# Performance work log

Measured on AMD Instinct MI355X. Metric: run time of the kernel, lower is better.

The kernel has to match this reference:

```python
import jax, jax.numpy as jnp
import numpy as np

# Static graph layout: B equal-sized graphs so per-graph k is constant (jit-friendly).
NUM_GRAPHS = 128
NODES_PER_GRAPH = 1024
NUM_NODES = NUM_GRAPHS * NODES_PER_GRAPH  # 131072
NUM_EDGES = NUM_NODES * 32               # 4194304
CHANNELS = 256
RATIO = 0.5
K = max(1, int(NODES_PER_GRAPH * RATIO))  # 512, matches max(1, int(count*ratio))


def setup_inputs() -> dict:
    key = jax.random.key(0)
    k0, k1, k2, k3 = jax.random.split(key, 4)
    x = jax.random.normal(k0, (NUM_NODES, CHANNELS), dtype=jnp.float32)
    edge_index = jax.random.randint(k1, (2, NUM_EDGES), 0, NUM_NODES, dtype=jnp.int64)
    batch = (jnp.arange(NUM_NODES, dtype=jnp.int64) // NODES_PER_GRAPH)
    # score MLP params: Linear(C, C) -> tanh -> Linear(C, 1)
    s = 1.0 / np.sqrt(CHANNELS)
    W1 = jax.random.uniform(k2, (CHANNELS, CHANNELS), jnp.float32, -s, s)
    b1 = jnp.zeros((CHANNELS,), jnp.float32)
    W2 = jax.random.uniform(k3, (CHANNELS, 1), jnp.float32, -s, s)
    b2 = jnp.zeros((1,), jnp.float32)
    return {"x": x, "edge_index": edge_index, "batch": batch,
            "W1": W1, "b1": b1, "W2": W2, "b2": b2}


def reference(x, edge_index, batch, W1, b1, W2, b2):
    # Note: SAGPool.forward computes a GNN score then discards it and calls
    # super().forward, which recomputes scores with the self.score MLP. The GNN
    # path is dead code (and would error in torch); the effective math is below.
    scores = (jnp.tanh(x @ W1 + b1) @ W2 + b2)[:, 0]  # [num_nodes]

    # Per-graph top-k, vectorized across all graphs (equal-sized segments).
    s = scores.reshape(NUM_GRAPHS, NODES_PER_GRAPH)
    top_s, top_i = jax.lax.top_k(s, K)  # descending per graph, matches torch.topk
    offsets = (jnp.arange(NUM_GRAPHS, dtype=top_i.dtype) * NODES_PER_GRAPH)[:, None]
    perm = (top_i + offsets).reshape(-1)  # [B*K] global indices, graphs in order

    x_pooled = x[perm]
    batch_pooled = batch[perm]
    scores_pooled = top_s.reshape(-1)

    # Edge filtering: keep edges whose both endpoints survive.
    keep = jnp.zeros((NUM_NODES,), dtype=bool).at[perm].set(True)
    row, col = edge_index
    edge_mask = keep[row] & keep[col]
    # Static-shape compaction: stable-sort kept edges to the front, pad with -1.
    order = jnp.argsort(~edge_mask, stable=True)
    edge_index_pooled = jnp.where(edge_mask[order][None, :], edge_index[:, order], -1)

    return x_pooled, edge_index_pooled, batch_pooled, perm, scores_pooled
```

## Files before the change

kernel.cpp:

```cpp
#include <hip/hip_runtime.h>
#include <hip/hip_bf16.h>

#define NG 128
#define NPG 1024
#define NN (NG * NPG)
#define NE (NN * 32)
#define CH 256
#define KSEL 512

#define CAP 128
#define EPS 0.02f

#define OUT_X      0
#define OUT_EDGE   16777216
#define OUT_BATCH  25165824
#define OUT_PERM   25231360
#define OUT_SCORES 25296896

#define WS_SCORES  0
#define WS_KEEP    524288
#define WS_COUNTS  540672
#define WS_OFFSETS 544768
#define WS_BFRAG   548864
#define WS_BIDX    679936
#define WS_BSCORE  745472
#define WS_BN      811008
#define WS_BLO     811520

typedef __attribute__((ext_vector_type(8))) short bf16x8;
typedef __attribute__((ext_vector_type(4))) float f32x4;

__device__ __forceinline__ unsigned short f2bf(float f) {
    unsigned int b = __float_as_uint(f);
    return (unsigned short)((b + 0x7fffu + ((b >> 16) & 1u)) >> 16);
}

__device__ __forceinline__ float tanh_fast(float h) {
    const float e = __expf(2.0f * h);
    return 1.0f - 2.0f / (e + 1.0f);
}

__global__ __launch_bounds__(256)
void k_cvtW(const float* __restrict__ W1, unsigned short* __restrict__ W1b,
            unsigned int* __restrict__ keep_bits)
{
    const int t = blockIdx.x * 256 + threadIdx.x;
    if (t < NN / 32) keep_bits[t] = 0u;
    const int s    = t >> 10;
    const int rem  = t & 1023;
    const int n    = rem >> 6;
    const int lane = rem & 63;
    const int kbase = s * 32 + (lane >> 4) * 8;
    const int col   = n * 16 + (lane & 15);
    unsigned short u[8];
    #pragma unroll
    for (int j = 0; j < 8; ++j)
        u[j] = f2bf(W1[(size_t)(kbase + j) * CH + col]);
    uint4 v;
    v.x = u[0] | ((unsigned int)u[1] << 16);
    v.y = u[2] | ((unsigned int)u[3] << 16);
    v.z = u[4] | ((unsigned int)u[5] << 16);
    v.w = u[6] | ((unsigned int)u[7] << 16);
    *(uint4*)&W1b[(size_t)t * 8] = v;
}

__global__ __launch_bounds__(256, 3)
void k_mfma_scores(const float* __restrict__ x, const unsigned short* __restrict__ W1b,
                   const float* __restrict__ b1, const float* __restrict__ W2,
                   const float* __restrict__ b2, float* __restrict__ scores)
{
    __shared__ __align__(16) float Xf[2][2048];
    __shared__ float epi[4][64];

    const int tid = threadIdx.x;
    const int w_  = tid >> 6;
    const int l   = tid & 63;
    const int n0  = blockIdx.x * 64;

    #define STAGEX(c_, b_)                                                          \
    do {                                                                            \
        _Pragma("unroll")                                                           \
        for (int i = 0; i < 2; ++i) {                                               \
            const int G   = i * 256 + tid;                  \
            const int row = G >> 3;                                                 \
            const int gl  = (G & 7) ^ (row & 7);        \
            const float* src = x + (size_t)(n0 + row) * CH + (c_) * 32 + gl * 4;    \
            float* lb = &Xf[b_][0] + i * 1024 + w_ * 256;    \
            __builtin_amdgcn_global_load_lds(                                       \
                (const __attribute__((address_space(1))) void*)src,                 \
                (__attribute__((address_space(3))) void*)lb, 16, 0, 0);             \
        }                                                                           \
    } while (0)

    f32x4 acc[4][4];
    #pragma unroll
    for (int m = 0; m < 4; ++m)
        #pragma unroll
        for (int n = 0; n < 4; ++n)
            acc[m][n] = (f32x4){0.f, 0.f, 0.f, 0.f};

    const unsigned short* Wl = W1b + l * 8;
    bf16x8 bc[4], bn[4];
    #pragma unroll
    for (int ni = 0; ni < 4; ++ni)
        bc[ni] = *(const bf16x8*)&Wl[(size_t)(w_ * 4 + ni) * 512];

    STAGEX(0, 0);
    __syncthreads();

    #pragma unroll
    for (int s = 0; s < 8; ++s) {
        if (s < 7) STAGEX(s + 1, (s + 1) & 1);

        if (s < 7) {
            #pragma unroll
            for (int ni = 0; ni < 4; ++ni)
                bn[ni] = *(const bf16x8*)&Wl[(size_t)((s + 1) * 16 + w_ * 4 + ni) * 512];
        }

        const char* Xc = (const char*)&Xf[s & 1][0];
        bf16x8 a[4];
        #pragma unroll
        for (int m = 0; m < 4; ++m) {
            const int row = m * 16 + (l & 15);
            const int sw  = row & 7;
            const int g0  = (l >> 4) * 2;
            const float4 f0 = *(const float4*)(Xc + row * 128 + ((g0 ^ sw) << 4));
            const float4 f1 = *(const float4*)(Xc + row * 128 + (((g0 + 1) ^ sw) << 4));
            union { bf16x8 v; __hip_bfloat162 h[4]; } ua;
            ua.h[0] = __float22bfloat162_rn(make_float2(f0.x, f0.y));
            ua.h[1] = __float22bfloat162_rn(make_float2(f0.z, f0.w));
            ua.h[2] = __float22bfloat162_rn(make_float2(f1.x, f1.y));
            ua.h[3] = __float22bfloat162_rn(make_float2(f1.z, f1.w));
            a[m] = ua.v;
        }
        #pragma unroll
        for (int ni = 0; ni < 4; ++ni)
            #pragma unroll
            for (int m = 0; m < 4; ++m)
                acc[m][ni] = __builtin_amdgcn_mfma_f32_16x16x32_bf16(a[m], bc[ni], acc[m][ni], 0, 0, 0);
        #pragma unroll
        for (int ni = 0; ni < 4; ++ni) bc[ni] = bn[ni];

        __syncthreads();
    }
    #undef STAGEX

    float part[16];
    #pragma unroll
    for (int i = 0; i < 16; ++i) part[i] = 0.f;
    #pragma unroll
    for (int ni = 0; ni < 4; ++ni) {
        const int col = w_ * 64 + ni * 16 + (l & 15);
        const float b1c = b1[col];
        const float w2c = W2[col];
        #pragma unroll
        for (int m = 0; m < 4; ++m)
            #pragma unroll
            for (int r = 0; r < 4; ++r)
                part[m * 4 + r] += tanh_fast(acc[m][ni][r] + b1c) * w2c;
    }
    #pragma unroll
    for (int off = 1; off < 16; off <<= 1)
        #pragma unroll
        for (int i = 0; i < 16; ++i)
            part[i] += __shfl_xor(part[i], off, 64);

    if ((l & 15) == 0) {
        const int gq = l >> 4;
        #pragma unroll
        for (int m = 0; m < 4; ++m)
            #pragma unroll
            for (int r = 0; r < 4; ++r)
                epi[w_][m * 16 + gq * 4 + r] = part[m * 4 + r];
    }
    __syncthreads();
    if (tid < 64)
        scores[n0 + tid] = epi[0][tid] + epi[1][tid] + epi[2][tid] + epi[3][tid] + b2[0];
}

__global__ __launch_bounds__(512)
void k_topk(const float* __restrict__ scores, float* __restrict__ out,
            unsigned int* __restrict__ keep_bits, int* __restrict__ band_idx,
            int* __restrict__ band_n, int* __restrict__ band_lo)
{
    __shared__ float sv[1024];
    __shared__ int   si[1024];
    __shared__ int   s_lo, s_hi;
    const int g = blockIdx.x;
    const int t = threadIdx.x;
    sv[t]       = scores[g * NPG + t];       si[t]       = t;
    sv[t + 512] = scores[g * NPG + t + 512]; si[t + 512] = t + 512;

    for (int size = 2; size <= 1024; size <<= 1) {
        for (int stride = size >> 1; stride > 0; stride >>= 1) {
            __syncthreads();
            const int lo = ((t & ~(stride - 1)) << 1) | (t & (stride - 1));
            const int hi = lo + stride;
            const bool dirDesc = ((lo & size) == 0);
            const float va = sv[lo], vb = sv[hi];
            const int ia = si[lo], ib = si[hi];
            const bool aB = (va > vb) || (va == vb && ia < ib);
            if (aB != dirDesc) {
                sv[lo] = vb; sv[hi] = va;
                si[lo] = ib; si[hi] = ia;
            }
        }
    }
    __syncthreads();
    if (t == 0) { s_hi = 1024; }
    __syncthreads();
    const float tau = sv[511];
    if (sv[t] <= tau + EPS && (t == 0 || sv[t - 1] > tau + EPS)) s_lo = t;
    {
        const int p2 = t + 512;
        if (sv[p2] < tau - EPS && sv[p2 - 1] >= tau - EPS) s_hi = p2;
    }
    __syncthreads();
    const int lo = s_lo;
    const int bn = min(s_hi - lo, CAP);

    const int gi = g * NPG + si[t];
    out[OUT_BATCH + g * KSEL + t] = (float)g;
    if (t < lo) {
        out[OUT_PERM   + g * KSEL + t] = (float)gi;
        out[OUT_SCORES + g * KSEL + t] = sv[t];
        atomicOr(&keep_bits[gi >> 5], 1u << (gi & 31));
    }
    if (t < CAP)
        band_idx[g * CAP + t] = (t < bn) ? si[lo + t] : 0;
    if (t == 0) { band_n[g] = bn; band_lo[g] = lo; }
}

__global__ __launch_bounds__(256, 2)
void k_rescore(const float* __restrict__ x, const float* __restrict__ W1,
               const float* __restrict__ b1, const float* __restrict__ W2,
               const float* __restrict__ b2, const int* __restrict__ band_idx,
               const int* __restrict__ band_n, float* __restrict__ band_scores)
{
    const int g = blockIdx.x >> 2;
    const int c0 = (blockIdx.x & 3) * 32;
    if (band_n[g] <= c0) return;

    __shared__ __align__(16) float W1s[16][CH];
    __shared__ __align__(16) float Xs[32][16];

    const int tid = threadIdx.x;
    const int w_  = tid >> 6;
    const int l   = tid & 63;

    int iv = 0;
    if (w_ < 2) iv = band_idx[g * CAP + c0 + w_ * 16 + (l >> 2)] & 1023;
    const float* xg = x + ((size_t)g * NPG + iv) * CH;

    const float4 b1v = *(const float4*)&b1[l * 4];
    float acc[8][4];
    #pragma unroll
    for (int n = 0; n < 8; ++n) {
        acc[n][0] = b1v.x; acc[n][1] = b1v.y; acc[n][2] = b1v.z; acc[n][3] = b1v.w;
    }

    for (int kc = 0; kc < 16; ++kc) {
        __syncthreads();
        #pragma unroll
        for (int it = 0; it < 4; ++it) {
            const float* gp = W1 + (size_t)kc * (16 * CH) + (w_ * 4 + it) * CH + l * 4;
            float* lb = &W1s[0][0] + (w_ * 4 + it) * CH;
            __builtin_amdgcn_global_load_lds(
                (const __attribute__((address_space(1))) void*)gp,
                (__attribute__((address_space(3))) void*)lb, 16, 0, 0);
        }
        if (w_ < 2) {
            const float* gp = xg + kc * 16 + (l & 3) * 4;
            float* lb = &Xs[0][0] + w_ * 256;
            __builtin_amdgcn_global_load_lds(
                (const __attribute__((address_space(1))) void*)gp,
                (__attribute__((address_space(3))) void*)lb, 16, 0, 0);
        }
        __syncthreads();

        #pragma unroll
        for (int kq = 0; kq < 4; ++kq) {
            const int k4 = kq * 4;
            const float4 wv0 = *(const float4*)&W1s[k4 + 0][l * 4];
            const float4 wv1 = *(const float4*)&W1s[k4 + 1][l * 4];
            const float4 wv2 = *(const float4*)&W1s[k4 + 2][l * 4];
            const float4 wv3 = *(const float4*)&W1s[k4 + 3][l * 4];
            #pragma unroll
            for (int n = 0; n < 8; ++n) {
                const float4 xv = *(const float4*)&Xs[w_ * 8 + n][k4];
                acc[n][0] = fmaf(xv.x, wv0.x, acc[n][0]);
                acc[n][1] = fmaf(xv.x, wv0.y, acc[n][1]);
                acc[n][2] = fmaf(xv.x, wv0.z, acc[n][2]);
                acc[n][3] = fmaf(xv.x, wv0.w, acc[n][3]);
                acc[n][0] = fmaf(xv.y, wv1.x, acc[n][0]);
                acc[n][1] = fmaf(xv.y, wv1.y, acc[n][1]);
                acc[n][2] = fmaf(xv.y, wv1.z, acc[n][2]);
                acc[n][3] = fmaf(xv.y, wv1.w, acc[n][3]);
                acc[n][0] = fmaf(xv.z, wv2.x, acc[n][0]);
                acc[n][1] = fmaf(xv.z, wv2.y, acc[n][1]);
                acc[n][2] = fmaf(xv.z, wv2.z, acc[n][2]);
                acc[n][3] = fmaf(xv.z, wv2.w, acc[n][3]);
                acc[n][0] = fmaf(xv.w, wv3.x, acc[n][0]);
                acc[n][1] = fmaf(xv.w, wv3.y, acc[n][1]);
                acc[n][2] = fmaf(xv.w, wv3.z, acc[n][2]);
                acc[n][3] = fmaf(xv.w, wv3.w, acc[n][3]);
            }
        }
    }

    const float4 w2v = *(const float4*)&W2[l * 4];
    const float  bb  = b2[0];
    float s_[8];
    #pragma unroll
    for (int n = 0; n < 8; ++n) {
        s_[n] = tanhf(acc[n][0]) * w2v.x + tanhf(acc[n][1]) * w2v.y
              + tanhf(acc[n][2]) * w2v.z + tanhf(acc[n][3]) * w2v.w;
    }
    #pragma unroll
    for (int off = 1; off < 64; off <<= 1)
        #pragma unroll
        for (int n = 0; n < 8; ++n)
            s_[n] += __shfl_xor(s_[n], off, 64);

    if (l == 0) {
        #pragma unroll
        for (int n = 0; n < 8; ++n)
            band_scores[g * CAP + c0 + w_ * 8 + n] = s_[n] + bb;
    }
}

__global__ __launch_bounds__(64)
void k_bandsel(const float* __restrict__ band_scores, const int* __restrict__ band_idx,
               const int* __restrict__ band_n, const int* __restrict__ band_lo,
               float* __restrict__ out, unsigned int* __restrict__ keep_bits)
{
    __shared__ float bs[CAP];
    __shared__ int   bi[CAP];
    const int g = blockIdx.x;
    const int t = threadIdx.x;
    const int n  = band_n[g];
    const int lo = band_lo[g];
    int needed = KSEL - lo;
    if (needed > n) needed = n;

    #pragma unroll
    for (int h = 0; h < 2; ++h) {
        const int q = t + h * 64;
        const bool valid = q < n;
        bs[q] = valid ? band_scores[g * CAP + q] : -3.402823466e+38f;
        bi[q] = valid ? band_idx[g * CAP + q] : (NPG + q);
    }
    __syncthreads();
    for (int size = 2; size <= CAP; size <<= 1) {
        for (int stride = size >> 1; stride > 0; stride >>= 1) {
            __syncthreads();
            const int lo_i = ((t & ~(stride - 1)) << 1) | (t & (stride - 1));
            const int hi_i = lo_i + stride;
            const bool dirDesc = ((lo_i & size) == 0);
            const float va = bs[lo_i], vb = bs[hi_i];
            const int ia = bi[lo_i], ib = bi[hi_i];
            const bool aB = (va > vb) || (va == vb && ia < ib);
            if (aB != dirDesc) {
                bs[lo_i] = vb; bs[hi_i] = va;
                bi[lo_i] = ib; bi[hi_i] = ia;
            }
        }
    }
    __syncthreads();
    #pragma unroll
    for (int h = 0; h < 2; ++h) {
        const int s = t + h * 64;
        if (s < needed) {
            const int li = bi[s];
            const int gi = g * NPG + li;
            out[OUT_PERM   + g * KSEL + lo + s] = (float)gi;
            out[OUT_SCORES + g * KSEL + lo + s] = bs[s];
            atomicOr(&keep_bits[gi >> 5], 1u << (gi & 31));
        }
    }
}

__global__ __launch_bounds__(256)
void k_gather(const float* __restrict__ x, const float* __restrict__ perm_f,
              float* __restrict__ out_x)
{
    const int row  = blockIdx.x * 4 + (threadIdx.x >> 6);
    const int lane = threadIdx.x & 63;
    const int pi = (int)perm_f[row];
    const float4* src = (const float4*)&x[(size_t)pi * CH];
    float4* dst = (float4*)&out_x[(size_t)row * CH];
    dst[lane] = src[lane];
}

__global__ __launch_bounds__(256)
void k_edgecount(const int* __restrict__ ei, const unsigned int* __restrict__ keep_bits,
                 int* __restrict__ counts, float* __restrict__ out_edge)
{
    const int t = threadIdx.x;
    const float4 neg = make_float4(-1.f, -1.f, -1.f, -1.f);
    #pragma unroll
    for (int q = 0; q < 4; ++q) {
        ((float4*)out_edge)[(size_t)blockIdx.x * 1024 + q * 256 + t] = neg;
        ((float4*)(out_edge + NE))[(size_t)blockIdx.x * 1024 + q * 256 + t] = neg;
    }

    const size_t base = (size_t)blockIdx.x * 4096 + (size_t)t * 16;
    const int* rowp = ei;
    const int* colp = ei + NE;
    int rv[16], cv[16];
    #pragma unroll
    for (int q = 0; q < 4; ++q) {
        int4 r4 = *(const int4*)&rowp[base + q * 4];
        int4 c4 = *(const int4*)&colp[base + q * 4];
        rv[q*4+0]=r4.x; rv[q*4+1]=r4.y; rv[q*4+2]=r4.z; rv[q*4+3]=r4.w;
        cv[q*4+0]=c4.x; cv[q*4+1]=c4.y; cv[q*4+2]=c4.z; cv[q*4+3]=c4.w;
    }
    int cnt = 0;
    #pragma unroll
    for (int q = 0; q < 16; ++q)
        cnt += (int)((keep_bits[rv[q] >> 5] >> (rv[q] & 31)) &
                     (keep_bits[cv[q] >> 5] >> (cv[q] & 31)) & 1u);

    #pragma unroll
    for (int off = 1; off < 64; off <<= 1) cnt += __shfl_xor(cnt, off, 64);
    __shared__ int wsum[4];
    if ((t & 63) == 0) wsum[t >> 6] = cnt;
    __syncthreads();
    if (t == 0) counts[blockIdx.x] = wsum[0] + wsum[1] + wsum[2] + wsum[3];
}

__global__ __launch_bounds__(1024)
void k_scan(const int* __restrict__ counts, int* __restrict__ offsets)
{
    __shared__ int tmp[1024];
    const int t = threadIdx.x;
    const int c = counts[t];
    tmp[t] = c;
    __syncthreads();
    for (int off = 1; off < 1024; off <<= 1) {
        int v = (t >= off) ? tmp[t - off] : 0;
        __syncthreads();
        tmp[t] += v;
        __syncthreads();
    }
    offsets[t] = tmp[t] - c;
}

__global__ __launch_bounds__(256)
void k_scatter(const int* __restrict__ ei, const unsigned int* __restrict__ keep_bits,
               const int* __restrict__ offsets, float* __restrict__ out_edge)
{
    const int t = threadIdx.x;
    const size_t base = (size_t)blockIdx.x * 4096 + (size_t)t * 16;
    const int* rowp = ei;
    const int* colp = ei + NE;
    int rv[16], cv[16];
    #pragma unroll
    for (int q = 0; q < 4; ++q) {
        int4 r4 = *(const int4*)&rowp[base + q * 4];
        int4 c4 = *(const int4*)&colp[base + q * 4];
        rv[q*4+0]=r4.x; rv[q*4+1]=r4.y; rv[q*4+2]=r4.z; rv[q*4+3]=r4.w;
        cv[q*4+0]=c4.x; cv[q*4+1]=c4.y; cv[q*4+2]=c4.z; cv[q*4+3]=c4.w;
    }
    unsigned m = 0; int cnt = 0;
    #pragma unroll
    for (int q = 0; q < 16; ++q) {
        const bool kk = ((keep_bits[rv[q] >> 5] >> (rv[q] & 31)) &
                         (keep_bits[cv[q] >> 5] >> (cv[q] & 31)) & 1u) != 0u;
        m |= ((unsigned)kk) << q;
        cnt += (int)kk;
    }
    const int lane = t & 63, w = t >> 6;
    int incl = cnt;
    #pragma unroll
    for (int off = 1; off < 64; off <<= 1) {
        int v = __shfl_up(incl, off, 64);
        if (lane >= off) incl += v;
    }
    __shared__ int wtot[4];
    if (lane == 63) wtot[w] = incl;
    __syncthreads();
    int wbase = 0;
    for (int i = 0; i < w; ++i) wbase += wtot[i];
    int pos = offsets[blockIdx.x] + wbase + (incl - cnt);
    #pragma unroll
    for (int q = 0; q < 16; ++q) {
        if (m & (1u << q)) {
            out_edge[pos]      = (float)rv[q];
            out_edge[NE + pos] = (float)cv[q];
            ++pos;
        }
    }
}

extern "C" void kernel_launch(void* const* d_in, const int* in_sizes, int n_in,
                              void* d_out, int out_size, void* d_ws, size_t ws_size,
                              hipStream_t stream)
{
    const float* x  = (const float*)d_in[0];
    const int*   ei = (const int*)d_in[1];
    const float* W1 = (const float*)d_in[3];
    const float* b1 = (const float*)d_in[4];
    const float* W2 = (const float*)d_in[5];
    const float* b2 = (const float*)d_in[6];

    float* out = (float*)d_out;
    char*  ws  = (char*)d_ws;
    float*          scores    = (float*)(ws + WS_SCORES);
    unsigned int*   keep_bits = (unsigned int*)(ws + WS_KEEP);
    int*            counts    = (int*)(ws + WS_COUNTS);
    int*            offsets   = (int*)(ws + WS_OFFSETS);
    unsigned short* W1b       = (unsigned short*)(ws + WS_BFRAG);
    int*            band_idx  = (int*)(ws + WS_BIDX);
    float*          band_sc   = (float*)(ws + WS_BSCORE);
    int*            band_n    = (int*)(ws + WS_BN);
    int*            band_lo   = (int*)(ws + WS_BLO);

    k_cvtW<<<32, 256, 0, stream>>>(W1, W1b, keep_bits);
    k_mfma_scores<<<NN / 64, 256, 0, stream>>>(x, W1b, b1, W2, b2, scores);
    k_topk<<<NG, 512, 0, stream>>>(scores, out, keep_bits, band_idx, band_n, band_lo);
    k_rescore<<<NG * (CAP / 32), 256, 0, stream>>>(x, W1, b1, W2, b2, band_idx, band_n, band_sc);
    k_bandsel<<<NG, 64, 0, stream>>>(band_sc, band_idx, band_n, band_lo, out, keep_bits);
    k_gather<<<(NG * KSEL) / 4, 256, 0, stream>>>(x, out + OUT_PERM, out + OUT_X);
    k_edgecount<<<NE / 4096, 256, 0, stream>>>(ei, keep_bits, counts, out + OUT_EDGE);
    k_scan<<<1, 1024, 0, stream>>>(counts, offsets);
    k_scatter<<<NE / 4096, 256, 0, stream>>>(ei, keep_bits, offsets, out + OUT_EDGE);
}
```

Baseline: 165.8 us.

## Restructure score GEMM so each wave owns 16 rows across all columns

```diff
diff --git a/kernel.cpp b/kernel.cpp
--- a/kernel.cpp
+++ b/kernel.cpp
@@ -69,114 +69,60 @@
                    const float* __restrict__ b1, const float* __restrict__ W2,
                    const float* __restrict__ b2, float* __restrict__ scores)
 {
-    __shared__ __align__(16) float Xf[2][2048];
-    __shared__ float epi[4][64];
-
     const int tid = threadIdx.x;
     const int w_  = tid >> 6;
     const int l   = tid & 63;
     const int n0  = blockIdx.x * 64;
 
-    #define STAGEX(c_, b_)                                                          \
-    do {                                                                            \
-        _Pragma("unroll")                                                           \
-        for (int i = 0; i < 2; ++i) {                                               \
-            const int G   = i * 256 + tid;                  \
-            const int row = G >> 3;                                                 \
-            const int gl  = (G & 7) ^ (row & 7);        \
-            const float* src = x + (size_t)(n0 + row) * CH + (c_) * 32 + gl * 4;    \
-            float* lb = &Xf[b_][0] + i * 1024 + w_ * 256;    \
-            __builtin_amdgcn_global_load_lds(                                       \
-                (const __attribute__((address_space(1))) void*)src,                 \
-                (__attribute__((address_space(3))) void*)lb, 16, 0, 0);             \
-        }                                                                           \
-    } while (0)
-
-    f32x4 acc[4][4];
-    #pragma unroll
-    for (int m = 0; m < 4; ++m)
-        #pragma unroll
-        for (int n = 0; n < 4; ++n)
-            acc[m][n] = (f32x4){0.f, 0.f, 0.f, 0.f};
+    const int arow = n0 + w_ * 16 + (l & 15);
+    const float* xr = x + (size_t)arow * CH + (l >> 4) * 8;
+
+    f32x4 acc[16];
+    #pragma unroll
+    for (int nt = 0; nt < 16; ++nt) acc[nt] = (f32x4){0.f, 0.f, 0.f, 0.f};
 
     const unsigned short* Wl = W1b + l * 8;
-    bf16x8 bc[4], bn[4];
-    #pragma unroll
-    for (int ni = 0; ni < 4; ++ni)
-        bc[ni] = *(const bf16x8*)&Wl[(size_t)(w_ * 4 + ni) * 512];
-
-    STAGEX(0, 0);
-    __syncthreads();
 
     #pragma unroll
     for (int s = 0; s < 8; ++s) {
-        if (s < 7) STAGEX(s + 1, (s + 1) & 1);
-
-        if (s < 7) {
-            #pragma unroll
-            for (int ni = 0; ni < 4; ++ni)
-                bn[ni] = *(const bf16x8*)&Wl[(size_t)((s + 1) * 16 + w_ * 4 + ni) * 512];
-        }
-
-        const char* Xc = (const char*)&Xf[s & 1][0];
-        bf16x8 a[4];
-        #pragma unroll
-        for (int m = 0; m < 4; ++m) {
-            const int row = m * 16 + (l & 15);
-            const int sw  = row & 7;
-            const int g0  = (l >> 4) * 2;
-            const float4 f0 = *(const float4*)(Xc + row * 128 + ((g0 ^ sw) << 4));
-            const float4 f1 = *(const float4*)(Xc + row * 128 + (((g0 + 1) ^ sw) << 4));
-            union { bf16x8 v; __hip_bfloat162 h[4]; } ua;
-            ua.h[0] = __float22bfloat162_rn(make_float2(f0.x, f0.y));
-            ua.h[1] = __float22bfloat162_rn(make_float2(f0.z, f0.w));
-            ua.h[2] = __float22bfloat162_rn(make_float2(f1.x, f1.y));
-            ua.h[3] = __float22bfloat162_rn(make_float2(f1.z, f1.w));
-            a[m] = ua.v;
-        }
-        #pragma unroll
-        for (int ni = 0; ni < 4; ++ni)
-            #pragma unroll
-            for (int m = 0; m < 4; ++m)
-                acc[m][ni] = __builtin_amdgcn_mfma_f32_16x16x32_bf16(a[m], bc[ni], acc[m][ni], 0, 0, 0);
-        #pragma unroll
-        for (int ni = 0; ni < 4; ++ni) bc[ni] = bn[ni];
-
-        __syncthreads();
-    }
-    #undef STAGEX
-
-    float part[16];
-    #pragma unroll
-    for (int i = 0; i < 16; ++i) part[i] = 0.f;
-    #pragma unroll
-    for (int ni = 0; ni < 4; ++ni) {
-        const int col = w_ * 64 + ni * 16 + (l & 15);
+        const float4 f0 = *(const float4*)(xr + s * 32);
+        const float4 f1 = *(const float4*)(xr + s * 32 + 4);
+        union { bf16x8 v; __hip_bfloat162 h[4]; } ua;
+        ua.h[0] = __float22bfloat162_rn(make_float2(f0.x, f0.y));
+        ua.h[1] = __float22bfloat162_rn(make_float2(f0.z, f0.w));
+        ua.h[2] = __float22bfloat162_rn(make_float2(f1.x, f1.y));
+        ua.h[3] = __float22bfloat162_rn(make_float2(f1.z, f1.w));
+        const bf16x8 a = ua.v;
+        #pragma unroll
+        for (int nt = 0; nt < 16; ++nt) {
+            const bf16x8 b = *(const bf16x8*)&Wl[(size_t)(s * 16 + nt) * 512];
+            acc[nt] = __builtin_amdgcn_mfma_f32_16x16x32_bf16(a, b, acc[nt], 0, 0, 0);
+        }
+    }
+
+    float part[4] = {0.f, 0.f, 0.f, 0.f};
+    #pragma unroll
+    for (int nt = 0; nt < 16; ++nt) {
+        const int col = nt * 16 + (l & 15);
         const float b1c = b1[col];
         const float w2c = W2[col];
         #pragma unroll
-        for (int m = 0; m < 4; ++m)
-            #pragma unroll
-            for (int r = 0; r < 4; ++r)
-                part[m * 4 + r] += tanh_fast(acc[m][ni][r] + b1c) * w2c;
+        for (int r = 0; r < 4; ++r)
+            part[r] += tanh_fast(acc[nt][r] + b1c) * w2c;
     }
     #pragma unroll
     for (int off = 1; off < 16; off <<= 1)
         #pragma unroll
-        for (int i = 0; i < 16; ++i)
-            part[i] += __shfl_xor(part[i], off, 64);
+        for (int r = 0; r < 4; ++r)
+            part[r] += __shfl_xor(part[r], off, 64);
 
     if ((l & 15) == 0) {
-        const int gq = l >> 4;
-        #pragma unroll
-        for (int m = 0; m < 4; ++m)
-            #pragma unroll
-            for (int r = 0; r < 4; ++r)
-                epi[w_][m * 16 + gq * 4 + r] = part[m * 4 + r];
-    }
-    __syncthreads();
-    if (tid < 64)
-        scores[n0 + tid] = epi[0][tid] + epi[1][tid] + epi[2][tid] + epi[3][tid] + b2[0];
+        const float bb = b2[0];
+        const int rbase = n0 + w_ * 16 + (l >> 4) * 4;
+        #pragma unroll
+        for (int r = 0; r < 4; ++r)
+            scores[rbase + r] = part[r] + bb;
+    }
 }
 
 __global__ __launch_bounds__(512)
```

Result: slower. 187.3 us (+13.0%).
